# Kernel tuning notes

Hardware: AMD Instinct MI355X
Metric: run time of the kernel (lower is better)

Reference implementation:

```python
import jax, jax.numpy as jnp
import numpy as np
from math import sqrt

D_MODEL = 768
N_HEADS = 12
D_K = 64
D_V = 64
LN_EPS = 1e-5
NEG = -1e9


def layer_norm(x, g, b):
    mu = jnp.mean(x, axis=-1, keepdims=True)
    var = jnp.mean((x - mu) ** 2, axis=-1, keepdims=True)
    return (x - mu) * jax.lax.rsqrt(var + LN_EPS) * g + b


def setup_inputs() -> dict:
    key = jax.random.key(0)
    ks = jax.random.split(key, 8)
    B, S = 4, 1024
    pro1 = jax.random.normal(ks[0], (B, S, D_MODEL), dtype=jnp.float32)
    pro2 = jax.random.normal(ks[1], (B, S, D_MODEL), dtype=jnp.float32)
    # attn_mask is [B, H, S2, S1]; transpose(2,3) masks scores [B,H,S1,S2]
    mask1_2 = jax.random.bernoulli(ks[2], 0.3, (B, N_HEADS, S, S))
    sc = 1.0 / np.sqrt(D_MODEL)
    W_Q = jax.random.normal(ks[3], (D_MODEL, D_K * N_HEADS), dtype=jnp.float32) * sc
    W_K = jax.random.normal(ks[4], (D_MODEL, D_K * N_HEADS), dtype=jnp.float32) * sc
    fc1 = jax.random.normal(ks[5], (D_V * N_HEADS, D_MODEL), dtype=jnp.float32) * sc
    g1 = jnp.ones((D_MODEL,), jnp.float32)
    b1 = jnp.zeros((D_MODEL,), jnp.float32)
    g2 = jnp.ones((D_MODEL,), jnp.float32)
    b2 = jnp.zeros((D_MODEL,), jnp.float32)
    return {"pro1": pro1, "pro2": pro2, "mask1_2": mask1_2,
            "W_Q": W_Q, "W_K": W_K, "fc1": fc1,
            "g1": g1, "b1": b1, "g2": g2, "b2": b2}


def reference(pro1, pro2, mask1_2, W_Q, W_K, fc1, g1, b1, g2, b2):
    B, S1, _ = pro1.shape
    S2 = pro2.shape[1]
    # project and split heads: [B, H, S, d_k]
    Q = (pro1 @ W_Q).reshape(B, S1, N_HEADS, D_K).transpose(0, 2, 1, 3)
    K = (pro2 @ W_K).reshape(B, S2, N_HEADS, D_K).transpose(0, 2, 1, 3)
    scores = jnp.einsum('bhsd,bhtd->bhst', Q, K) / sqrt(D_K)  # [B,H,S1,S2]
    mask = jnp.swapaxes(mask1_2, 2, 3)  # attn_mask.transpose(2,3)
    scores = jnp.where(mask, NEG, scores)
    attn1 = jax.nn.softmax(scores, axis=-1)                  # over S2
    attn2 = jax.nn.softmax(jnp.swapaxes(scores, -1, -2), axis=-1)  # over S1
    ctx1 = jnp.einsum('bhst,bhtd->bhsd', attn1, K)  # [B,H,S1,d_k]
    ctx2 = jnp.einsum('bhts,bhsd->bhtd', attn2, Q)  # [B,H,S2,d_k]
    c1 = ctx1.transpose(0, 2, 1, 3).reshape(B, S1, N_HEADS * D_V)
    c2 = ctx2.transpose(0, 2, 1, 3).reshape(B, S2, N_HEADS * D_V)
    # NOTE: original applies fc1 to BOTH branches (fc2 is dead code)
    o1 = layer_norm(c1 @ fc1, g1, b1)
    o2 = layer_norm(c2 @ fc1, g2, b2)
    return (o1, o2)
```

## Files before the change

kernel.cpp:

```cpp
#include <hip/hip_runtime.h>
#include <hip/hip_bf16.h>
#include <stdint.h>

#define S 1024
#define DMODEL 768
#define NH 12
#define DK 64
#define BB 4
#define BH 48
#define M4 4096

typedef __attribute__((ext_vector_type(8))) short bf16x8;
typedef __attribute__((ext_vector_type(4))) float f32x4;
typedef __attribute__((ext_vector_type(4))) _Float16 f16x4;
typedef __attribute__((ext_vector_type(8))) _Float16 f16x8;

static __device__ __forceinline__ unsigned short f2bf(float f) {
  unsigned int u = __float_as_uint(f);
  unsigned int r = u + 0x7FFFu + ((u >> 16) & 1u);
  return (unsigned short)(r >> 16);
}
static __device__ __forceinline__ unsigned pkbf(float a, float b) {
  unsigned r;
  asm("v_cvt_pk_bf16_f32 %0, %1, %2" : "=v"(r) : "v"(a), "v"(b));
  return r;
}
static __device__ __forceinline__ bf16x8 ldfrag(const unsigned short* p) {
  uint4 q = *reinterpret_cast<const uint4*>(p);
  return __builtin_bit_cast(bf16x8, q);
}
static __device__ __forceinline__ f16x8 ldfragh(const unsigned short* p) {
  uint4 q = *reinterpret_cast<const uint4*>(p);
  return __builtin_bit_cast(f16x8, q);
}
static __device__ __forceinline__ unsigned short h2u(_Float16 h) {
  return __builtin_bit_cast(unsigned short, h);
}
static __device__ __forceinline__ f16x4 pack4(const float* p) {
  auto lo = __builtin_amdgcn_cvt_pkrtz(p[0], p[1]);
  auto hi = __builtin_amdgcn_cvt_pkrtz(p[2], p[3]);
  uint2 u;
  u.x = __builtin_bit_cast(unsigned int, lo);
  u.y = __builtin_bit_cast(unsigned int, hi);
  return __builtin_bit_cast(f16x4, u);
}
static __device__ __forceinline__ float exp8(float x) {
#if __has_builtin(__builtin_amdgcn_exp2f)
  return __builtin_amdgcn_exp2f(x * 0.18033688011112042f);
#else
  return __expf(x * 0.125f);
#endif
}
static __device__ __forceinline__ void gl2lds16(const unsigned short* g, unsigned short* l) {
  __builtin_amdgcn_global_load_lds(
      (const __attribute__((address_space(1))) unsigned int*)g,
      (__attribute__((address_space(3))) unsigned int*)l, 16, 0, 0);
}

__global__ __launch_bounds__(256) void k_prep(const float* __restrict__ w0, const float* __restrict__ w1,
                                              const float* __restrict__ w2,
                                              unsigned short* __restrict__ o0, unsigned short* __restrict__ o1,
                                              unsigned short* __restrict__ o2) {
  int bid = blockIdx.x;
  int tid = threadIdx.x;
  int z = bid / 576;
  int r2 = bid - z * 576;
  int bx = r2 % 24, by = r2 / 24;
  const float* in = z == 0 ? w0 : (z == 1 ? w1 : w2);
  unsigned short* out = z == 0 ? o0 : (z == 1 ? o1 : o2);
  __shared__ float tile[32][33];
  int n0 = bx * 32, k0 = by * 32;
  int r = tid >> 3, c = (tid & 7) * 4;
  float4 v = *reinterpret_cast<const float4*>(in + (size_t)(k0 + r) * DMODEL + n0 + c);
  tile[r][c] = v.x; tile[r][c + 1] = v.y; tile[r][c + 2] = v.z; tile[r][c + 3] = v.w;
  __syncthreads();
  ushort4 o;
  o.x = f2bf(tile[c + 0][r]);
  o.y = f2bf(tile[c + 1][r]);
  o.z = f2bf(tile[c + 2][r]);
  o.w = f2bf(tile[c + 3][r]);
  *reinterpret_cast<ushort4*>(out + (size_t)(n0 + r) * DMODEL + k0 + c) = o;
}

__global__ __launch_bounds__(256, 3) void k_g0p(
    const float* __restrict__ Af0, const float* __restrict__ Af1,
    const unsigned short* __restrict__ Bt0, const unsigned short* __restrict__ Bt1,
    unsigned short* __restrict__ oQ0, unsigned short* __restrict__ oQ1,
    unsigned short* __restrict__ oT0, unsigned short* __restrict__ oT1,
    const int* __restrict__ mask, unsigned int* __restrict__ mp2) {
  int grpb = blockIdx.x >> 3, t8 = blockIdx.x & 7;
  int lin = (grpb >> 1) * 8 + t8;
  int tid = threadIdx.x;

  if (grpb & 1) {
    int bh = lin >> 4;
    int px = lin & 15;
    int w = tid >> 6, lane = tid & 63;
    int tile4 = px * 4 + w;
    int rowg = tile4 >> 2, colg = tile4 & 3;
    int t0 = rowg * 64;
    const int* mb = mask + (size_t)bh * S * S + colg * 256;
    unsigned long long b0 = 0, b1 = 0, b2 = 0, b3 = 0;
#pragma unroll 8
    for (int r = 0; r < 64; ++r) {
      int4 v = *reinterpret_cast<const int4*>(mb + (size_t)(t0 + r) * S + lane * 4);
      unsigned long long c0 = __ballot(v.x != 0);
      unsigned long long c1 = __ballot(v.y != 0);
      unsigned long long c2 = __ballot(v.z != 0);
      unsigned long long c3 = __ballot(v.w != 0);
      if (lane == r) { b0 = c0; b1 = c1; b2 = c2; b3 = c3; }
    }
    unsigned int* p2 = mp2 + (size_t)bh * 32 * S + (size_t)(colg * 8) * S + t0 + lane;
    p2[(size_t)0 * S] = (unsigned)b0;  p2[(size_t)1 * S] = (unsigned)(b0 >> 32);
    p2[(size_t)2 * S] = (unsigned)b1;  p2[(size_t)3 * S] = (unsigned)(b1 >> 32);
    p2[(size_t)4 * S] = (unsigned)b2;  p2[(size_t)5 * S] = (unsigned)(b2 >> 32);
    p2[(size_t)6 * S] = (unsigned)b3;  p2[(size_t)7 * S] = (unsigned)(b3 >> 32);
    return;
  }

  int z = lin / 384;
  int rr = lin - z * 384;
  int nb = rr % 6, mbp = rr / 6;
  int m0 = mbp * 64, n0 = nb * 128;
  const unsigned short* Bt = z ? Bt1 : Bt0;
  __shared__ __align__(16) unsigned short As[64 * 64];
  __shared__ __align__(16) unsigned short Bs[128 * 64];
  int w = tid >> 6, lane = tid & 63, lane15 = lane & 15, quad = lane >> 4;
  int col0 = w * 32;
  f32x4 acc[4][2] = {};

  const unsigned short* gB[4];
  unsigned short* lB[4];
  {
    int lr = lane >> 3, ch = lane & 7;
#pragma unroll
    for (int i = 0; i < 4; ++i) {
      int r = w * 32 + i * 8 + lr;
      int cs = ((ch ^ (r & 7)) * 8);
      gB[i] = Bt + (size_t)(n0 + r) * DMODEL + cs;
      lB[i] = &Bs[(w * 32 + i * 8) * 64];
    }
  }
  int ar = tid >> 2, aj0 = (tid & 3) * 2;
  const float* gAf = (z ? Af1 : Af0) + (size_t)(m0 + ar) * DMODEL + aj0 * 8;
  float4 af[4];
#pragma unroll
  for (int q = 0; q < 4; ++q) af[q] = *reinterpret_cast<const float4*>(gAf + q * 4);
  int arx = ar & 7;
  unsigned short* lAw0 = &As[ar * 64 + ((aj0 ^ arx) * 8)];
  unsigned short* lAw1 = &As[ar * 64 + (((aj0 + 1) ^ arx) * 8)];

#pragma unroll
  for (int i = 0; i < 4; ++i) gl2lds16(gB[i], lB[i]);
  {
    uint4 w0, w1;
    w0.x = pkbf(af[0].x, af[0].y); w0.y = pkbf(af[0].z, af[0].w);
    w0.z = pkbf(af[1].x, af[1].y); w0.w = pkbf(af[1].z, af[1].w);
    w1.x = pkbf(af[2].x, af[2].y); w1.y = pkbf(af[2].z, af[2].w);
    w1.z = pkbf(af[3].x, af[3].y); w1.w = pkbf(af[3].z, af[3].w);
    *reinterpret_cast<uint4*>(lAw0) = w0;
    *reinterpret_cast<uint4*>(lAw1) = w1;
  }

  int l7 = lane15 & 7;
  for (int kc = 0; kc < 12; ++kc) {
    __syncthreads();
    if (kc < 11) {
#pragma unroll
      for (int q = 0; q < 4; ++q)
        af[q] = *reinterpret_cast<const float4*>(gAf + (kc + 1) * 64 + q * 4);
    }
#pragma unroll
    for (int ks = 0; ks < 2; ++ks) {
      int co = (((ks * 4 + quad) ^ l7) * 8);
      bf16x8 a[4], b[2];
#pragma unroll
      for (int i = 0; i < 4; ++i) a[i] = ldfrag(&As[(i * 16 + lane15) * 64 + co]);
#pragma unroll
      for (int j = 0; j < 2; ++j) b[j] = ldfrag(&Bs[(col0 + j * 16 + lane15) * 64 + co]);
#pragma unroll
      for (int i = 0; i < 4; ++i)
#pragma unroll
        for (int j = 0; j < 2; ++j)
          acc[i][j] = __builtin_amdgcn_mfma_f32_16x16x32_bf16(a[i], b[j], acc[i][j], 0, 0, 0);
    }
    __syncthreads();
    if (kc < 11) {
      int ko = (kc + 1) * 64;
#pragma unroll
      for (int i = 0; i < 4; ++i) gl2lds16(gB[i] + ko, lB[i]);
      uint4 w0, w1;
      w0.x = pkbf(af[0].x, af[0].y); w0.y = pkbf(af[0].z, af[0].w);
      w0.z = pkbf(af[1].x, af[1].y); w0.w = pkbf(af[1].z, af[1].w);
      w1.x = pkbf(af[2].x, af[2].y); w1.y = pkbf(af[2].z, af[2].w);
      w1.z = pkbf(af[3].x, af[3].y); w1.w = pkbf(af[3].z, af[3].w);
      *reinterpret_cast<uint4*>(lAw0) = w0;
      *reinterpret_cast<uint4*>(lAw1) = w1;
    }
  }

  unsigned short* out = z ? oQ1 : oQ0;
  unsigned short* outT = z ? oT1 : oT0;
  f16x4 iden;
#pragma unroll
  for (int i = 0; i < 4; ++i) iden[i] = (_Float16)((quad * 4 + i) == lane15 ? 1.0f : 0.0f);
  f32x4 zero4 = {};
#pragma unroll
  for (int i = 0; i < 4; ++i)
#pragma unroll
    for (int j = 0; j < 2; ++j) {
      f16x4 cf;
#pragma unroll
      for (int reg = 0; reg < 4; ++reg) cf[reg] = (_Float16)acc[i][j][reg];
      f32x4 tq = __builtin_amdgcn_mfma_f32_16x16x16f16(cf, iden, zero4, 0, 0, 0);
      {
        int m = m0 + i * 16 + lane15;
        int n = n0 + col0 + j * 16 + quad * 4;
        int b = m >> 10, s = m & 1023, h = n >> 6, d = n & 63;
        ushort4 o;
        o.x = h2u((_Float16)tq[0]); o.y = h2u((_Float16)tq[1]);
        o.z = h2u((_Float16)tq[2]); o.w = h2u((_Float16)tq[3]);
        *reinterpret_cast<ushort4*>(&out[(((size_t)(b * NH + h)) * S + s) * DK + d]) = o;
      }
      {
        int n = n0 + col0 + j * 16 + lane15;
        int m = m0 + i * 16 + quad * 4;
        int b = m >> 10, s = m & 1023, h = n >> 6, d = n & 63;
        ushort4 o;
        o.x = h2u((_Float16)acc[i][j][0]); o.y = h2u((_Float16)acc[i][j][1]);
        o.z = h2u((_Float16)acc[i][j][2]); o.w = h2u((_Float16)acc[i][j][3]);
        *reinterpret_cast<ushort4*>(&outT[(((size_t)(b * NH + h)) * DK + d) * S + s]) = o;
      }
    }
}

__global__ __launch_bounds__(256, 3) void k_gemm1(
    const unsigned short* __restrict__ A0, const unsigned short* __restrict__ A1,
    const unsigned short* __restrict__ Bt,
    unsigned short* __restrict__ oH0, unsigned short* __restrict__ oH1) {
  int lin = blockIdx.x;
  int z = lin / 384;
  int rr = lin - z * 384;
  int nb = rr % 6, mbp = rr / 6;
  int m0 = mbp * 64, n0 = nb * 128;
  const unsigned short* A = z ? A1 : A0;
  __shared__ __align__(16) unsigned short As[64 * 64];
  __shared__ __align__(16) unsigned short Bs[128 * 64];
  int tid = threadIdx.x;
  int w = tid >> 6, lane = tid & 63, lane15 = lane & 15, quad = lane >> 4;
  int col0 = w * 32;
  f32x4 acc[4][2] = {};

  const unsigned short* gB[4];
  unsigned short* lB[4];
  const unsigned short* gA[2];
  unsigned short* lA[2];
  {
    int lr = lane >> 3, ch = lane & 7;
#pragma unroll
    for (int i = 0; i < 4; ++i) {
      int r = w * 32 + i * 8 + lr;
      int cs = ((ch ^ (r & 7)) * 8);
      gB[i] = Bt + (size_t)(n0 + r) * DMODEL + cs;
      lB[i] = &Bs[(w * 32 + i * 8) * 64];
    }
#pragma unroll
    for (int i = 0; i < 2; ++i) {
      int r = w * 16 + i * 8 + lr;
      int cs = ((ch ^ (r & 7)) * 8);
      gA[i] = A + (size_t)(m0 + r) * DMODEL + cs;
      lA[i] = &As[(w * 16 + i * 8) * 64];
    }
  }
#pragma unroll
  for (int i = 0; i < 4; ++i) gl2lds16(gB[i], lB[i]);
#pragma unroll
  for (int i = 0; i < 2; ++i) gl2lds16(gA[i], lA[i]);

  int l7 = lane15 & 7;
  for (int kc = 0; kc < 12; ++kc) {
    __syncthreads();
#pragma unroll
    for (int ks = 0; ks < 2; ++ks) {
      int co = (((ks * 4 + quad) ^ l7) * 8);
      bf16x8 a[4], b[2];
#pragma unroll
      for (int i = 0; i < 4; ++i) a[i] = ldfrag(&As[(i * 16 + lane15) * 64 + co]);
#pragma unroll
      for (int j = 0; j < 2; ++j) b[j] = ldfrag(&Bs[(col0 + j * 16 + lane15) * 64 + co]);
#pragma unroll
      for (int i = 0; i < 4; ++i)
#pragma unroll
        for (int j = 0; j < 2; ++j)
          acc[i][j] = __builtin_amdgcn_mfma_f32_16x16x32_bf16(a[i], b[j], acc[i][j], 0, 0, 0);
    }
    __syncthreads();
    if (kc < 11) {
      int ko = (kc + 1) * 64;
#pragma unroll
      for (int i = 0; i < 4; ++i) gl2lds16(gB[i] + ko, lB[i]);
#pragma unroll
      for (int i = 0; i < 2; ++i) gl2lds16(gA[i] + ko, lA[i]);
    }
  }

  unsigned short* outh = z ? oH1 : oH0;
#pragma unroll
  for (int i = 0; i < 4; ++i)
#pragma unroll
    for (int j = 0; j < 2; ++j)
#pragma unroll
      for (int reg = 0; reg < 4; ++reg) {
        int m = m0 + i * 16 + quad * 4 + reg;
        int n = n0 + col0 + j * 16 + lane15;
        outh[(size_t)m * DMODEL + n] = h2u((_Float16)acc[i][j][reg]);
      }
}

__global__ __launch_bounds__(256, 3) void k_attn(
    const unsigned short* __restrict__ Qb, const unsigned short* __restrict__ Kb,
    const unsigned short* __restrict__ QT, const unsigned short* __restrict__ KT,
    const unsigned int* __restrict__ mp2,
    unsigned short* __restrict__ c1, unsigned short* __restrict__ c2) {
  int lin = blockIdx.x;
  int xcd = lin & 7, idx = lin >> 3;
  int grp = xcd * 12 + (idx >> 3);
  int sb = idx & 7;
  int path = grp >= 48 ? 1 : 0;
  int bh = grp - path * 48;
  int s0b = sb * 128;

  const unsigned short* X = path ? Kb : Qb;
  const unsigned short* Y = path ? Qb : Kb;
  const unsigned short* YT = path ? QT : KT;
  unsigned short* outc = path ? c2 : c1;

  __shared__ __align__(16) unsigned short YS[2][64 * 72];
  __shared__ __align__(16) unsigned short YTS[2][64 * 72];
  __shared__ __align__(16) unsigned int MWS[2][512];

  const unsigned short* Xb = X + (size_t)bh * S * DK;
  const unsigned short* Yb = Y + (size_t)bh * S * DK;
  const unsigned short* YTb = YT + (size_t)bh * DK * S;
  const unsigned int* mbg = mp2 + (size_t)bh * 32 * S;

  int tid = threadIdx.x;
  int w = tid >> 6, lane = tid & 63, lane15 = lane & 15, quad = lane >> 4;
  int s0w = s0b + w * 32;
  int ck = lane15 & 3;
  int sh0 = w * 8 + (lane15 >> 2);

  f16x8 xf[2][2];
#pragma unroll
  for (int rg = 0; rg < 2; ++rg) {
    xf[rg][0] = ldfragh(Xb + (size_t)(s0w + rg * 16 + lane15) * DK + quad * 8);
    xf[rg][1] = ldfragh(Xb + (size_t)(s0w + rg * 16 + lane15) * DK + 32 + quad * 8);
  }

  int sr4 = tid >> 2, sc4 = (tid & 3) * 16;
  const unsigned short* gY = Yb + (size_t)sr4 * DK + sc4;
  const unsigned short* gYT = YTb + (size_t)sr4 * S + sc4;
  uint4 y0 = *reinterpret_cast<const uint4*>(gY);
  uint4 y1 = *reinterpret_cast<const uint4*>(gY + 8);
  uint4 t0 = *reinterpret_cast<const uint4*>(gYT);
  uint4 t1 = *reinterpret_cast<const uint4*>(gYT + 8);

  int mj = tid >> 2;
  int p0wi = (sb >> 1) * 8 + (tid & 3) * 2 + (sb & 1);
  int tl = tid >> 1;
  int k0 = (tid & 1) * 2, k1 = k0 + 1;
  unsigned mwv0, mwv1 = 0;
  if (path == 0) {
    mwv0 = mbg[(size_t)p0wi * S + mj];
  } else {
    mwv0 = mbg[(size_t)(k0 * 2) * S + s0b + tl];
    mwv1 = mbg[(size_t)(k1 * 2) * S + s0b + tl];
  }

  f32x4 outa[2][4] = {};
  f32x4 outs[2] = {};
  f16x4 onesf;
#pragma unroll
  for (int i = 0; i < 4; ++i) onesf[i] = (_Float16)1.0f;

  for (int jc = 0; jc < 16; ++jc) {
    int buf = jc & 1;
    *reinterpret_cast<uint4*>(&YS[buf][sr4 * 72 + sc4]) = y0;
    *reinterpret_cast<uint4*>(&YS[buf][sr4 * 72 + sc4 + 8]) = y1;
    *reinterpret_cast<uint4*>(&YTS[buf][sr4 * 72 + sc4]) = t0;
    *reinterpret_cast<uint4*>(&YTS[buf][sr4 * 72 + sc4 + 8]) = t1;
    if (path == 0) {
      MWS[buf][tid] = mwv0;
    } else {
      uint2 mw; mw.x = mwv0; mw.y = mwv1;
      *reinterpret_cast<uint2*>(&MWS[buf][tid * 2]) = mw;
    }
    {
      int jcn = (jc + 1 < 16) ? jc + 1 : jc;
      int jn = jcn * 64;
      y0 = *reinterpret_cast<const uint4*>(gY + (size_t)jn * DK);
      y1 = *reinterpret_cast<const uint4*>(gY + (size_t)jn * DK + 8);
      t0 = *reinterpret_cast<const uint4*>(gYT + jn);
      t1 = *reinterpret_cast<const uint4*>(gYT + jn + 8);
      if (path == 0) {
        mwv0 = mbg[(size_t)p0wi * S + jn + mj];
      } else {
        size_t wb = (size_t)((jcn >> 2) * 8 + ((jcn >> 1) & 1)) * S + s0b + tl;
        mwv0 = mbg[wb + (size_t)(k0 * 2) * S];
        mwv1 = mbg[wb + (size_t)(k1 * 2) * S];
      }
    }
    __syncthreads();

    f32x4 scv[4][2];
    __builtin_amdgcn_s_setprio(1);
#pragma unroll
    for (int st = 0; st < 4; ++st) {
      f16x8 a0 = ldfragh(&YS[buf][(st * 16 + lane15) * 72 + quad * 8]);
      f16x8 a1 = ldfragh(&YS[buf][(st * 16 + lane15) * 72 + 32 + quad * 8]);
#pragma unroll
      for (int rg = 0; rg < 2; ++rg) {
        f32x4 v = {};
        v = __builtin_amdgcn_mfma_f32_16x16x32_f16(a0, xf[rg][0], v, 0, 0, 0);
        v = __builtin_amdgcn_mfma_f32_16x16x32_f16(a1, xf[rg][1], v, 0, 0, 0);
        scv[st][rg] = v;
      }
    }
    __builtin_amdgcn_s_setprio(0);
    f16x4 pfa[4][2];
    if (path == 0) {
#pragma unroll
      for (int st = 0; st < 4; ++st) {
        float pv[2][4];
#pragma unroll
        for (int reg = 0; reg < 4; ++reg) {
          unsigned wdv = MWS[buf][(st * 16 + quad * 4 + reg) * 4 + ck];
#pragma unroll
          for (int rg = 0; rg < 2; ++rg) {
            float e = exp8(scv[st][rg][reg]);
            pv[rg][reg] = ((wdv >> (unsigned)(sh0 + rg * 4)) & 1u) ? 0.f : e;
          }
        }
        pfa[st][0] = pack4(pv[0]);
        pfa[st][1] = pack4(pv[1]);
      }
    } else {
#pragma unroll
      for (int rg = 0; rg < 2; ++rg) {
        int bidx = (w * 32 + rg * 16 + lane15) * 4;
        uint4 wq = *reinterpret_cast<const uint4*>(&MWS[buf][bidx]);
        unsigned wd4[4] = {wq.x, wq.y, wq.z, wq.w};
#pragma unroll
        for (int st = 0; st < 4; ++st) {
          float pv[4];
          unsigned shb = (unsigned)((jc & 1) * 16 + st * 4 + quad);
#pragma unroll
          for (int reg = 0; reg < 4; ++reg) {
            float e = exp8(scv[st][rg][reg]);
            pv[reg] = ((wd4[reg] >> shb) & 1u) ? 0.f : e;
          }
          pfa[st][rg] = pack4(pv);
        }
      }
    }
    __builtin_amdgcn_s_setprio(1);
#pragma unroll
    for (int st = 0; st < 4; ++st) {
#pragma unroll
      for (int dsub = 0; dsub < 4; ++dsub) {
        uint2 q = *reinterpret_cast<const uint2*>(&YTS[buf][(dsub * 16 + lane15) * 72 + st * 16 + quad * 4]);
        f16x4 yb = __builtin_bit_cast(f16x4, q);
#pragma unroll
        for (int rg = 0; rg < 2; ++rg)
          outa[rg][dsub] = __builtin_amdgcn_mfma_f32_16x16x16f16(pfa[st][rg], yb, outa[rg][dsub], 0, 0, 0);
      }
#pragma unroll
      for (int rg = 0; rg < 2; ++rg)
        outs[rg] = __builtin_amdgcn_mfma_f32_16x16x16f16(pfa[st][rg], onesf, outs[rg], 0, 0, 0);
    }
    __builtin_amdgcn_s_setprio(0);
  }

  float rinv[2][4];
#pragma unroll
  for (int rg = 0; rg < 2; ++rg)
#pragma unroll
    for (int reg = 0; reg < 4; ++reg)
      rinv[rg][reg] = 1.0f / outs[rg][reg];

  int b = bh / NH, h = bh % NH;
#pragma unroll
  for (int rg = 0; rg < 2; ++rg)
#pragma unroll
    for (int dsub = 0; dsub < 4; ++dsub)
#pragma unroll
      for (int reg = 0; reg < 4; ++reg) {
        float v = outa[rg][dsub][reg] * rinv[rg][reg];
        int srow = s0w + rg * 16 + quad * 4 + reg;
        size_t idxo = ((size_t)(b * S) + srow) * DMODEL + h * DK + dsub * 16 + lane15;
        outc[idxo] = f2bf(v);
      }
}

__global__ __launch_bounds__(256) void k_ln(const unsigned short* __restrict__ f1,
                                            const unsigned short* __restrict__ f2,
                                            const float* __restrict__ g1, const float* __restrict__ b1,
                                            const float* __restrict__ g2, const float* __restrict__ b2,
                                            float* __restrict__ out) {
  int tid = threadIdx.x;
  int w = tid >> 6, lane = tid & 63;
  int rowg = blockIdx.x * 4 + w;
  int sel = rowg >> 12;
  int row = rowg & 4095;
  const unsigned short* p = (sel ? f2 : f1) + (size_t)row * DMODEL;
  const float* g = sel ? g2 : g1;
  const float* be = sel ? b2 : b1;

  float x[12];
#pragma unroll
  for (int k = 0; k < 3; ++k) {
    ushort4 v = *reinterpret_cast<const ushort4*>(p + k * 256 + lane * 4);
    x[k * 4 + 0] = (float)__builtin_bit_cast(_Float16, v.x);
    x[k * 4 + 1] = (float)__builtin_bit_cast(_Float16, v.y);
    x[k * 4 + 2] = (float)__builtin_bit_cast(_Float16, v.z);
    x[k * 4 + 3] = (float)__builtin_bit_cast(_Float16, v.w);
  }
  float s = 0.f, ss = 0.f;
#pragma unroll
  for (int i = 0; i < 12; ++i) { s += x[i]; ss += x[i] * x[i]; }
#pragma unroll
  for (int m = 1; m < 64; m <<= 1) { s += __shfl_xor(s, m); ss += __shfl_xor(ss, m); }
  float mu = s * (1.0f / 768.0f);
  float var = ss * (1.0f / 768.0f) - mu * mu;
  float rstd = rsqrtf(var + 1e-5f);

  float* o = out + ((size_t)sel * M4 + row) * DMODEL;
#pragma unroll
  for (int k = 0; k < 3; ++k) {
    float4 gv = *reinterpret_cast<const float4*>(g + k * 256 + lane * 4);
    float4 bv = *reinterpret_cast<const float4*>(be + k * 256 + lane * 4);
    float4 ov;
    ov.x = (x[k * 4 + 0] - mu) * rstd * gv.x + bv.x;
    ov.y = (x[k * 4 + 1] - mu) * rstd * gv.y + bv.y;
    ov.z = (x[k * 4 + 2] - mu) * rstd * gv.z + bv.z;
    ov.w = (x[k * 4 + 3] - mu) * rstd * gv.w + bv.w;
    *reinterpret_cast<float4*>(o + k * 256 + lane * 4) = ov;
  }
}

extern "C" void kernel_launch(void* const* d_in, const int* in_sizes, int n_in,
                              void* d_out, int out_size, void* d_ws, size_t ws_size,
                              hipStream_t stream) {
  const float* pro1 = (const float*)d_in[0];
  const float* pro2 = (const float*)d_in[1];
  const int* mask = (const int*)d_in[2];
  const float* WQ = (const float*)d_in[3];
  const float* WK = (const float*)d_in[4];
  const float* FC1 = (const float*)d_in[5];
  const float* g1 = (const float*)d_in[6];
  const float* b1 = (const float*)d_in[7];
  const float* g2 = (const float*)d_in[8];
  const float* b2 = (const float*)d_in[9];
  float* out = (float*)d_out;
  char* ws = (char*)d_ws;

  unsigned short* f1h = (unsigned short*)(ws + 0);
  unsigned short* wqt = (unsigned short*)(ws + 12582912);
  unsigned short* wkt = (unsigned short*)(ws + 13762560);
  unsigned short* fc1t = (unsigned short*)(ws + 14942208);
  unsigned short* Qb = (unsigned short*)(ws + 16121856);
  unsigned short* Kb = (unsigned short*)(ws + 22413312);
  unsigned short* QT = (unsigned short*)(ws + 28704768);
  unsigned short* KT = (unsigned short*)(ws + 34996224);
  unsigned int* mp2 = (unsigned int*)(ws + 41287680);
  unsigned short* f2h = (unsigned short*)(ws + 47579136);
  unsigned short* c1 = (unsigned short*)(ws + 60162048);
  unsigned short* c2 = (unsigned short*)(ws + 66453504);

  k_prep<<<1728, 256, 0, stream>>>(WQ, WK, FC1, wqt, wkt, fc1t);
  k_g0p<<<1536, 256, 0, stream>>>(pro1, pro2, wqt, wkt, Qb, Kb, QT, KT, mask, mp2);
  k_attn<<<dim3(768), 256, 0, stream>>>(Qb, Kb, QT, KT, mp2, c1, c2);
  k_gemm1<<<768, 256, 0, stream>>>(c1, c2, fc1t, f1h, f2h);
  k_ln<<<2048, 256, 0, stream>>>(f1h, f2h, g1, b1, g2, b2, out);
}
```

Measured before the change: 401.1 us.

## Move fc1 weight transpose into attention kernel tail, vectorize context stores via MFMA transpose

```diff
diff --git a/kernel.cpp b/kernel.cpp
--- a/kernel.cpp
+++ b/kernel.cpp
@@ -58,16 +58,14 @@
 }
 
 __global__ __launch_bounds__(256) void k_prep(const float* __restrict__ w0, const float* __restrict__ w1,
-                                              const float* __restrict__ w2,
-                                              unsigned short* __restrict__ o0, unsigned short* __restrict__ o1,
-                                              unsigned short* __restrict__ o2) {
+                                              unsigned short* __restrict__ o0, unsigned short* __restrict__ o1) {
   int bid = blockIdx.x;
   int tid = threadIdx.x;
   int z = bid / 576;
   int r2 = bid - z * 576;
   int bx = r2 % 24, by = r2 / 24;
-  const float* in = z == 0 ? w0 : (z == 1 ? w1 : w2);
-  unsigned short* out = z == 0 ? o0 : (z == 1 ? o1 : o2);
+  const float* in = z == 0 ? w0 : w1;
+  unsigned short* out = z == 0 ? o0 : o1;
   __shared__ float tile[32][33];
   int n0 = bx * 32, k0 = by * 32;
   int r = tid >> 3, c = (tid & 7) * 4;
@@ -321,8 +319,29 @@
     const unsigned short* __restrict__ Qb, const unsigned short* __restrict__ Kb,
     const unsigned short* __restrict__ QT, const unsigned short* __restrict__ KT,
     const unsigned int* __restrict__ mp2,
-    unsigned short* __restrict__ c1, unsigned short* __restrict__ c2) {
+    unsigned short* __restrict__ c1, unsigned short* __restrict__ c2,
+    const float* __restrict__ fcw, unsigned short* __restrict__ fct) {
   int lin = blockIdx.x;
+  int tid = threadIdx.x;
+
+  if (lin >= 768) {
+    int r2 = lin - 768;
+    int bx = r2 % 24, by = r2 / 24;
+    __shared__ float ttile[32][33];
+    int n0 = bx * 32, k0 = by * 32;
+    int r = tid >> 3, c = (tid & 7) * 4;
+    float4 v = *reinterpret_cast<const float4*>(fcw + (size_t)(k0 + r) * DMODEL + n0 + c);
+    ttile[r][c] = v.x; ttile[r][c + 1] = v.y; ttile[r][c + 2] = v.z; ttile[r][c + 3] = v.w;
+    __syncthreads();
+    ushort4 o;
+    o.x = f2bf(ttile[c + 0][r]);
+    o.y = f2bf(ttile[c + 1][r]);
+    o.z = f2bf(ttile[c + 2][r]);
+    o.w = f2bf(ttile[c + 3][r]);
+    *reinterpret_cast<ushort4*>(fct + (size_t)(n0 + r) * DMODEL + k0 + c) = o;
+    return;
+  }
+
   int xcd = lin & 7, idx = lin >> 3;
   int grp = xcd * 12 + (idx >> 3);
   int sb = idx & 7;
@@ -344,7 +363,6 @@
   const unsigned short* YTb = YT + (size_t)bh * DK * S;
   const unsigned int* mbg = mp2 + (size_t)bh * 32 * S;
 
-  int tid = threadIdx.x;
   int w = tid >> 6, lane = tid & 63, lane15 = lane & 15, quad = lane >> 4;
   int s0w = s0b + w * 32;
   int ck = lane15 & 3;
@@ -488,18 +506,27 @@
     for (int reg = 0; reg < 4; ++reg)
       rinv[rg][reg] = 1.0f / outs[rg][reg];
 
+  f16x4 iden;
+#pragma unroll
+  for (int i = 0; i < 4; ++i) iden[i] = (_Float16)((quad * 4 + i) == lane15 ? 1.0f : 0.0f);
+  f32x4 zero4 = {};
   int b = bh / NH, h = bh % NH;
 #pragma unroll
-  for (int rg = 0; rg < 2; ++rg)
-#pragma unroll
-    for (int dsub = 0; dsub < 4; ++dsub)
-#pragma unroll
-      for (int reg = 0; reg < 4; ++reg) {
-        float v = outa[rg][dsub][reg] * rinv[rg][reg];
-        int srow = s0w + rg * 16 + quad * 4 + reg;
-        size_t idxo = ((size_t)(b * S) + srow) * DMODEL + h * DK + dsub * 16 + lane15;
-        outc[idxo] = f2bf(v);
-      }
+  for (int rg = 0; rg < 2; ++rg) {
+    int srow = s0w + rg * 16 + lane15;
+    unsigned short* orow = outc + ((size_t)(b * S) + srow) * DMODEL + h * DK;
+#pragma unroll
+    for (int dsub = 0; dsub < 4; ++dsub) {
+      f16x4 cf;
+#pragma unroll
+      for (int reg = 0; reg < 4; ++reg)
+        cf[reg] = (_Float16)(outa[rg][dsub][reg] * rinv[rg][reg]);
+      f32x4 tq = __builtin_amdgcn_mfma_f32_16x16x16f16(cf, iden, zero4, 0, 0, 0);
+      ushort4 o;
+      o.x = f2bf(tq[0]); o.y = f2bf(tq[1]); o.z = f2bf(tq[2]); o.w = f2bf(tq[3]);
+      *reinterpret_cast<ushort4*>(&orow[dsub * 16 + quad * 4]) = o;
+    }
+  }
 }
 
 __global__ __launch_bounds__(256) void k_ln(const unsigned short* __restrict__ f1,
@@ -577,9 +604,9 @@
   unsigned short* c1 = (unsigned short*)(ws + 60162048);
   unsigned short* c2 = (unsigned short*)(ws + 66453504);
 
-  k_prep<<<1728, 256, 0, stream>>>(WQ, WK, FC1, wqt, wkt, fc1t);
+  k_prep<<<1152, 256, 0, stream>>>(WQ, WK, wqt, wkt);
   k_g0p<<<1536, 256, 0, stream>>>(pro1, pro2, wqt, wkt, Qb, Kb, QT, KT, mask, mp2);
-  k_attn<<<dim3(768), 256, 0, stream>>>(Qb, Kb, QT, KT, mp2, c1, c2);
+  k_attn<<<dim3(1344), 256, 0, stream>>>(Qb, Kb, QT, KT, mp2, c1, c2, FC1, fc1t);
   k_gemm1<<<768, 256, 0, stream>>>(c1, c2, fc1t, f1h, f2h);
   k_ln<<<2048, 256, 0, stream>>>(f1h, f2h, g1, b1, g2, b2, out);
 }
```

After: 402.6 us. About the same (+0.4%).
